# Performance work log

Hardware: AMD Instinct MI355X
Metric: run time of the kernel (lower is better)

## Reference

```python
import jax, jax.numpy as jnp
import numpy as np

B, C, H, W = 2, 256, 64, 64
NH, HD, K = 4, 64, 16  # num_head, head_channel, n_clusters
N = H * W
SCALE = HD ** 0.5


def _lin(x, Wm, b):
    return x @ Wm + b


def _mlp(x, W1, b1, W2, b2):
    h = _lin(x, W1, b1)
    h = jnp.where(h > 0, h, 0.01 * h)  # LeakyReLU(0.01)
    return _lin(h, W2, b2)  # dropout p=0.0 -> identity


def setup_inputs() -> dict:
    key = jax.random.key(0)
    ks = jax.random.split(key, 20)
    s = 1.0 / np.sqrt(C)
    s2 = 1.0 / np.sqrt(2 * C)
    inp = {
        "q_img": jax.random.normal(ks[0], (B, C, H, W), jnp.float32),
        "k_img_map": jax.random.normal(ks[1], (B, C, H, W), jnp.float32),
        "v_img_map": jax.random.normal(ks[2], (B, C, H, W), jnp.float32),
        "labels": jax.random.randint(ks[3], (B, H, W), 0, K),
        "pixel_coefficients": jax.random.uniform(ks[4], (B, N, N), jnp.float32),
        "Wq": jax.random.uniform(ks[5], (C, C), jnp.float32, -s, s),
        "bq": jnp.zeros((C,), jnp.float32),
        "Wk": jax.random.uniform(ks[6], (C, C), jnp.float32, -s, s),
        "bk": jnp.zeros((C,), jnp.float32),
        "Wv": jax.random.uniform(ks[7], (C, C), jnp.float32, -s, s),
        "bv": jnp.zeros((C,), jnp.float32),
        "W11": jax.random.uniform(ks[8], (C, 2 * C), jnp.float32, -s, s),
        "b11": jnp.zeros((2 * C,), jnp.float32),
        "W12": jax.random.uniform(ks[9], (2 * C, C), jnp.float32, -s2, s2),
        "b12": jnp.zeros((C,), jnp.float32),
        "W21": jax.random.uniform(ks[10], (C, 2 * C), jnp.float32, -s, s),
        "b21": jnp.zeros((2 * C,), jnp.float32),
        "W22": jax.random.uniform(ks[11], (2 * C, C), jnp.float32, -s2, s2),
        "b22": jnp.zeros((C,), jnp.float32),
    }
    return inp


def reference(q_img, k_img_map, v_img_map, labels, pixel_coefficients,
              Wq, bq, Wk, bk, Wv, bv, W11, b11, W12, b12, W21, b21, W22, b22):
    # [B,C,H,W] -> [B,N,C]
    q = _lin(q_img.transpose(0, 2, 3, 1).reshape(B, N, C), Wq, bq)
    k = _lin(k_img_map.transpose(0, 2, 3, 1).reshape(B, N, C), Wk, bk)
    v = _lin(v_img_map.transpose(0, 2, 3, 1).reshape(B, N, C), Wv, bv)

    lab = labels.reshape(B, N)
    onehot = (lab[:, :, None] == jnp.arange(K)[None, None, :]).astype(jnp.float32)  # [B,N,K]
    num_k = jnp.einsum('bnk,bnc->bkc', onehot, k)
    den_k = onehot.sum(axis=1)[:, :, None] + 1e-6
    centers_k = num_k / den_k  # [B,K,C]

    qm = q.reshape(B, N, NH, HD).transpose(0, 2, 1, 3)  # [B,h,N,d]
    km = k.reshape(B, N, NH, HD).transpose(0, 2, 1, 3)
    vm = v.reshape(B, N, NH, HD).transpose(0, 2, 1, 3)
    cm = centers_k.reshape(B, K, NH, HD).transpose(0, 2, 1, 3)  # [B,h,K,d]

    attn_intra = jnp.einsum('bhnd,bhmd->bhnm', qm, km)          # [B,h,N,N]
    attn_centers = jnp.einsum('bhnd,bhkd->bhnk', qm, cm)        # [B,h,N,K]

    same = (lab[:, :, None] == lab[:, None, :])[:, None]        # [B,1,N,N]
    idx = jnp.broadcast_to(lab[:, None, None, :], (B, NH, N, N))
    attn_inter = jnp.take_along_axis(attn_centers, idx, axis=-1) * pixel_coefficients[:, None]

    scores = jnp.where(same, attn_intra, attn_inter) / SCALE
    attn = jax.nn.softmax(scores, axis=-1)
    out = jnp.einsum('bhnm,bhmd->bhnd', attn, vm).transpose(0, 2, 1, 3).reshape(B, N, C)

    rs1 = v + _mlp(out, W11, b11, W12, b12)        # [B,N,C] (v_spatial residual)
    rs2 = rs1 + _mlp(rs1, W21, b21, W22, b22)
    return rs2.reshape(B, H, W, C).transpose(0, 3, 1, 2)  # [B,C,H,W]
```

## Files before the change

### kernel.cpp

```cpp
#include <hip/hip_runtime.h>
#include <stdint.h>

#define Bv 2
#define Cv 256
#define Nv 4096
#define NHv 4
#define HDv 64
#define Kv 16


typedef __attribute__((ext_vector_type(8))) short bf16x8;
typedef __attribute__((ext_vector_type(4))) float f32x4;

__device__ __forceinline__ float bf2f(unsigned short u) {
  union { unsigned int i; float f; } x; x.i = ((unsigned int)u) << 16; return x.f;
}
__device__ __forceinline__ unsigned short f2bf(float f) {
  union { float f; unsigned int i; } x; x.f = f;
  unsigned int r = x.i + 0x7FFF + ((x.i >> 16) & 1);
  return (unsigned short)(r >> 16);
}

__global__ __launch_bounds__(256) void imgt_k(
    const float* __restrict__ qi, const float* __restrict__ ki,
    const float* __restrict__ vi, unsigned short* __restrict__ dst)
{
  const int z = blockIdx.z;
  const float* src = (z < 2 ? qi : (z < 4 ? ki : vi)) + (long long)(z & 1) * Cv * Nv;
  unsigned short* out = dst + (long long)z * Nv * Cv;
  __shared__ float t[32][33];
  const int x = threadIdx.x, y = threadIdx.y;
  const int n0 = blockIdx.x * 32, c0 = blockIdx.y * 32;
  for (int i = y; i < 32; i += 8)
    t[i][x] = src[(long long)(c0 + i) * Nv + n0 + x];
  __syncthreads();
  for (int i = y; i < 32; i += 8)
    out[(long long)(n0 + i) * Cv + c0 + x] = f2bf(t[x][i]);
}

struct WP { const float* p[7]; };

__global__ __launch_bounds__(256) void wt_k(WP wp, unsigned short* __restrict__ dst)
{
  const int z = blockIdx.z;
  const int KD[7] = {256, 256, 256, 256, 512, 256, 512};
  const int ND[7] = {256, 256, 256, 512, 256, 512, 256};
  const long long OFF[7] = {0, 65536, 131072, 196608, 327680, 458752, 589824};
  const int Kw = KD[z], Nw = ND[z];
  const int nb = blockIdx.x * 32, kb2 = blockIdx.y * 32;
  if (nb >= Nw || kb2 >= Kw) return;
  __shared__ float t[32][33];
  const int x = threadIdx.x, y = threadIdx.y;
  const float* src = wp.p[z];
  for (int i = y; i < 32; i += 8)
    t[i][x] = src[(long long)(kb2 + i) * Nw + nb + x];
  __syncthreads();
  for (int i = y; i < 32; i += 8)
    dst[OFF[z] + (long long)(nb + i) * Kw + kb2 + x] = f2bf(t[x][i]);
}

__global__ __launch_bounds__(256) void proj_k(
    const unsigned short* __restrict__ imgT, const unsigned short* __restrict__ wt,
    const float* __restrict__ bq, const float* __restrict__ bk, const float* __restrict__ bv,
    unsigned short* __restrict__ qbf, unsigned short* __restrict__ kbf,
    float* __restrict__ vpp, unsigned short* __restrict__ vtb)
{
  __shared__ __align__(16) unsigned short As[128][72];
  __shared__ __align__(16) unsigned short Bs[128][72];
  const int tid = threadIdx.x;
  const int w = tid >> 6, lane = tid & 63;
  const int lr = lane & 15, quad = lane >> 4;
  const int m0 = blockIdx.x * 128, n0 = blockIdx.y * 128;
  const int z = blockIdx.z, zz = z >> 1, bb = z & 1;
  const int wm = (w >> 1) * 64, wn = (w & 1) * 64;
  const int sr = tid >> 1, sh = (tid & 1) * 32;
  const long long NvCv = (long long)Nv * Cv;

  const float* bias = zz == 0 ? bq : (zz == 1 ? bk : bv);
  const unsigned short* Ab0 = imgT + (long long)z * NvCv + (long long)(m0 + sr) * Cv + sh;
  const unsigned short* Bb0 = wt + (long long)zz * 65536 + (long long)(n0 + sr) * Cv + sh;

  f32x4 acc[4][4];
#pragma unroll
  for (int i = 0; i < 4; ++i)
#pragma unroll
    for (int j = 0; j < 4; ++j) acc[i][j] = (f32x4){0.f, 0.f, 0.f, 0.f};

  for (int k0 = 0; k0 < Cv; k0 += 64) {
    const unsigned short* Ab = Ab0 + k0;
    const unsigned short* Bp = Bb0 + k0;
    uint4 a0 = *(const uint4*)Ab, a1 = *(const uint4*)(Ab + 8);
    uint4 a2 = *(const uint4*)(Ab + 16), a3 = *(const uint4*)(Ab + 24);
    uint4 b0 = *(const uint4*)Bp, b1 = *(const uint4*)(Bp + 8);
    uint4 b2 = *(const uint4*)(Bp + 16), b3 = *(const uint4*)(Bp + 24);
    *(uint4*)&As[sr][sh] = a0; *(uint4*)&As[sr][sh + 8] = a1;
    *(uint4*)&As[sr][sh + 16] = a2; *(uint4*)&As[sr][sh + 24] = a3;
    *(uint4*)&Bs[sr][sh] = b0; *(uint4*)&Bs[sr][sh + 8] = b1;
    *(uint4*)&Bs[sr][sh + 16] = b2; *(uint4*)&Bs[sr][sh + 24] = b3;
    __syncthreads();
#pragma unroll
    for (int ks = 0; ks < 2; ++ks) {
      bf16x8 af[4], bfr[4];
#pragma unroll
      for (int i = 0; i < 4; ++i)
        af[i] = *(const bf16x8*)&As[wm + i * 16 + lr][ks * 32 + quad * 8];
#pragma unroll
      for (int j = 0; j < 4; ++j)
        bfr[j] = *(const bf16x8*)&Bs[wn + j * 16 + lr][ks * 32 + quad * 8];
#pragma unroll
      for (int i = 0; i < 4; ++i)
#pragma unroll
        for (int j = 0; j < 4; ++j)
          acc[i][j] = __builtin_amdgcn_mfma_f32_16x16x32_bf16(af[i], bfr[j], acc[i][j], 0, 0, 0);
    }
    __syncthreads();
  }

#pragma unroll
  for (int j = 0; j < 4; ++j) {
    const int col = n0 + wn + j * 16 + lr;
    const float bvv = bias[col];
#pragma unroll
    for (int i = 0; i < 4; ++i) {
      const int mb = m0 + wm + i * 16 + quad * 4;
      float r[4];
#pragma unroll
      for (int reg = 0; reg < 4; ++reg) r[reg] = acc[i][j][reg] + bvv;
      const long long ob = (long long)bb * NvCv;
      if (zz == 0) {
#pragma unroll
        for (int reg = 0; reg < 4; ++reg)
          qbf[ob + (long long)(mb + reg) * Cv + col] = f2bf(r[reg] * 0.125f);
      } else if (zz == 1) {
#pragma unroll
        for (int reg = 0; reg < 4; ++reg)
          kbf[ob + (long long)(mb + reg) * Cv + col] = f2bf(r[reg]);
      } else {
#pragma unroll
        for (int reg = 0; reg < 4; ++reg)
          vpp[ob + (long long)(mb + reg) * Cv + col] = r[reg];
        uint2 pk;
        pk.x = f2bf(r[0]) | ((unsigned int)f2bf(r[1]) << 16);
        pk.y = f2bf(r[2]) | ((unsigned int)f2bf(r[3]) << 16);
        *(uint2*)&vtb[ob + (long long)col * Nv + mb] = pk;
      }
    }
  }
}

template<bool ABF16, int ACT, int RES, int OM>
__global__ __launch_bounds__(256) void mm_k(
    const void* __restrict__ A, const unsigned short* __restrict__ Bt,
    const float* __restrict__ bias, const float* __restrict__ Res,
    float* __restrict__ outF, unsigned short* __restrict__ outB,
    int M, int Nn, int Kd)
{
  __shared__ __align__(16) unsigned short As[128][72];
  __shared__ __align__(16) unsigned short Bs[128][72];
  const int tid = threadIdx.x;
  const int w = tid >> 6, lane = tid & 63;
  const int lr = lane & 15, quad = lane >> 4;
  const int m0 = blockIdx.x * 128, n0 = blockIdx.y * 128;
  const int wm = (w >> 1) * 64, wn = (w & 1) * 64;
  const int sr = tid >> 1, sh = (tid & 1) * 32;

  f32x4 acc[4][4];
#pragma unroll
  for (int i = 0; i < 4; ++i)
#pragma unroll
    for (int j = 0; j < 4; ++j) acc[i][j] = (f32x4){0.f, 0.f, 0.f, 0.f};

  const long long abase = (long long)(m0 + sr) * Kd + sh;
  const unsigned short* Bb = Bt + (long long)(n0 + sr) * Kd + sh;

  for (int k0 = 0; k0 < Kd; k0 += 64) {
    if (ABF16) {
      const unsigned short* Ab = (const unsigned short*)A + abase + k0;
      uint4 u0 = *(const uint4*)Ab, u1 = *(const uint4*)(Ab + 8);
      uint4 u2 = *(const uint4*)(Ab + 16), u3 = *(const uint4*)(Ab + 24);
      *(uint4*)&As[sr][sh] = u0; *(uint4*)&As[sr][sh + 8] = u1;
      *(uint4*)&As[sr][sh + 16] = u2; *(uint4*)&As[sr][sh + 24] = u3;
    } else {
      const float* Af = (const float*)A + abase + k0;
#pragma unroll
      for (int t = 0; t < 4; ++t) {
        const float4 f0 = *(const float4*)(Af + t * 8);
        const float4 f1 = *(const float4*)(Af + t * 8 + 4);
        uint4 pk;
        pk.x = f2bf(f0.x) | ((unsigned int)f2bf(f0.y) << 16);
        pk.y = f2bf(f0.z) | ((unsigned int)f2bf(f0.w) << 16);
        pk.z = f2bf(f1.x) | ((unsigned int)f2bf(f1.y) << 16);
        pk.w = f2bf(f1.z) | ((unsigned int)f2bf(f1.w) << 16);
        *(uint4*)&As[sr][sh + t * 8] = pk;
      }
    }
    {
      const unsigned short* Bp = Bb + k0;
      uint4 u0 = *(const uint4*)Bp, u1 = *(const uint4*)(Bp + 8);
      uint4 u2 = *(const uint4*)(Bp + 16), u3 = *(const uint4*)(Bp + 24);
      *(uint4*)&Bs[sr][sh] = u0; *(uint4*)&Bs[sr][sh + 8] = u1;
      *(uint4*)&Bs[sr][sh + 16] = u2; *(uint4*)&Bs[sr][sh + 24] = u3;
    }
    __syncthreads();
#pragma unroll
    for (int ks = 0; ks < 2; ++ks) {
      bf16x8 af[4], bfr[4];
#pragma unroll
      for (int i = 0; i < 4; ++i)
        af[i] = *(const bf16x8*)&As[wm + i * 16 + lr][ks * 32 + quad * 8];
#pragma unroll
      for (int j = 0; j < 4; ++j)
        bfr[j] = *(const bf16x8*)&Bs[wn + j * 16 + lr][ks * 32 + quad * 8];
#pragma unroll
      for (int i = 0; i < 4; ++i)
#pragma unroll
        for (int j = 0; j < 4; ++j)
          acc[i][j] = __builtin_amdgcn_mfma_f32_16x16x32_bf16(af[i], bfr[j], acc[i][j], 0, 0, 0);
    }
    __syncthreads();
  }

#pragma unroll
  for (int j = 0; j < 4; ++j) {
    const int col = n0 + wn + j * 16 + lr;
    const float bv = bias[col];
#pragma unroll
    for (int i = 0; i < 4; ++i) {
      const int mb = m0 + wm + i * 16 + quad * 4;
      float r[4];
#pragma unroll
      for (int reg = 0; reg < 4; ++reg) {
        float v = acc[i][j][reg] + bv;
        if (ACT) v = v > 0.f ? v : 0.01f * v;
        if (RES) v += Res[(long long)(mb + reg) * Nn + col];
        r[reg] = v;
      }
      if (OM == 0) {
#pragma unroll
        for (int reg = 0; reg < 4; ++reg)
          outF[(long long)(mb + reg) * Nn + col] = r[reg];
      } else if (OM == 1) {
#pragma unroll
        for (int reg = 0; reg < 4; ++reg)
          outB[(long long)(mb + reg) * Nn + col] = f2bf(r[reg]);
      } else {
        const float4 st = {r[0], r[1], r[2], r[3]};
        *(float4*)&outF[((long long)((mb >> 12) * Cv + col)) * Nv + (mb & 4095)] = st;
      }
    }
  }
}

__global__ __launch_bounds__(256) void zero_k(float* p, int n)
{
  const int i = blockIdx.x * 256 + threadIdx.x;
  if (i < n) p[i] = 0.f;
}

__global__ __launch_bounds__(256) void center_accum(
    const unsigned short* __restrict__ kb, const int* __restrict__ labels,
    float* __restrict__ cent, float* __restrict__ cnts)
{
  __shared__ int lab_s[512];
  const int bx = blockIdx.x;
  const int chunk = bx & 7;
  const int kk = (bx >> 3) & 15;
  const int b = bx >> 7;
  const int c = threadIdx.x;
  const int nbase = chunk * 512;
  for (int i = threadIdx.x; i < 512; i += 256) lab_s[i] = labels[b * Nv + nbase + i];
  __syncthreads();
  float acc = 0.f;
  int cnt = 0;
#pragma unroll 4
  for (int i = 0; i < 512; ++i) {
    if (lab_s[i] == kk) {
      acc += bf2f(kb[(long long)(b * Nv + nbase + i) * Cv + c]);
      ++cnt;
    }
  }
  atomicAdd(&cent[(b * Kv + kk) * Cv + c], acc);
  if (c == 0) atomicAdd(&cnts[b * Kv + kk], (float)cnt);
}

__global__ __launch_bounds__(256) void center_norm(float* cent, const float* cnts)
{
  const int i = blockIdx.x * 256 + threadIdx.x;
  cent[i] = cent[i] / (cnts[i >> 8] + 1e-6f);
}

union PSCS {
  unsigned short p[4][16][68];
  float c[16][68];
};

__global__ __launch_bounds__(256) void attn_k(
    const unsigned short* __restrict__ qb, const unsigned short* __restrict__ kb,
    const unsigned short* __restrict__ vtb, const float* __restrict__ cent,
    const int* __restrict__ labels, const float* __restrict__ pc,
    float* __restrict__ opart, float* __restrict__ lpart)
{
  __shared__ __align__(16) unsigned short q_s[64][72];
  __shared__ __align__(16) unsigned short k_s[64][72];
  __shared__ __align__(16) unsigned short vt_s[64][72];
  __shared__ __align__(16) PSCS u_s;
  __shared__ float ac_s[64][17];

  const int tid = threadIdx.x;
  const int lane = tid & 63, w = tid >> 6;
  const int lr = lane & 15, quad = lane >> 4;
  const int bx = blockIdx.x;
  const int qt = bx & 63, h = (bx >> 6) & 3, b = (bx >> 8) & 1;
  const int part = bx >> 9;
  const int n0 = qt * 64;
  const int mbase = part * 2048;
  const int sr2 = tid >> 2, so2 = (tid & 3) * 16;
  const int row_l = w * 16 + quad * 4;
  const long long pcb = (long long)b * Nv * Nv;

  {
    const unsigned short* src = qb + ((long long)(b * Nv + n0 + sr2)) * Cv + h * HDv + so2;
    *(uint4*)&q_s[sr2][so2] = *(const uint4*)src;
    *(uint4*)&q_s[sr2][so2 + 8] = *(const uint4*)(src + 8);
  }
  for (int idx = tid; idx < Kv * HDv; idx += 256)
    u_s.c[idx >> 6][idx & 63] = cent[((long long)(b * Kv + (idx >> 6))) * Cv + h * HDv + (idx & 63)];

  uint4 ka0, ka1, va0, va1;
  float pc1[4][4];
  int labm1[4], labq[4];
  {
    const long long ks = ((long long)(b * Nv + mbase + sr2)) * Cv + h * HDv + so2;
    ka0 = *(const uint4*)(kb + ks); ka1 = *(const uint4*)(kb + ks + 8);
    const long long vs = ((long long)(b * Cv + h * HDv + sr2)) * Nv + mbase + so2;
    va0 = *(const uint4*)(vtb + vs); va1 = *(const uint4*)(vtb + vs + 8);
  }
#pragma unroll
  for (int sub = 0; sub < 4; ++sub) {
    labm1[sub] = labels[b * Nv + mbase + sub * 16 + lr];
#pragma unroll
    for (int reg = 0; reg < 4; ++reg)
      pc1[sub][reg] = pc[pcb + (long long)(n0 + row_l + reg) * Nv + mbase + sub * 16 + lr];
  }
#pragma unroll
  for (int reg = 0; reg < 4; ++reg) labq[reg] = labels[b * Nv + n0 + row_l + reg];

  __syncthreads();
  for (int idx = tid; idx < 64 * Kv; idx += 256) {
    const int r = idx >> 4, kk = idx & 15;
    float s = 0.f;
#pragma unroll
    for (int d = 0; d < HDv; ++d) s += bf2f(q_s[r][d]) * u_s.c[kk][d];
    ac_s[r][kk] = s;
  }
  const bf16x8 qa0 = *(const bf16x8*)&q_s[w * 16 + lr][quad * 8];
  const bf16x8 qa1 = *(const bf16x8*)&q_s[w * 16 + lr][32 + quad * 8];
  __syncthreads();

  *(uint4*)&k_s[sr2][so2] = ka0; *(uint4*)&k_s[sr2][so2 + 8] = ka1;
  *(uint4*)&vt_s[sr2][so2] = va0; *(uint4*)&vt_s[sr2][so2 + 8] = va1;
  __syncthreads();

  f32x4 oacc[4];
#pragma unroll
  for (int s2 = 0; s2 < 4; ++s2) oacc[s2] = (f32x4){0.f, 0.f, 0.f, 0.f};
  float lrow[4] = {0.f, 0.f, 0.f, 0.f};

  for (int t = 0; t < 32; ++t) {
    const int m0 = mbase + t * 64;
    const bool has = (t < 31);

    if (has) {
      const long long ks = ((long long)(b * Nv + m0 + 64 + sr2)) * Cv + h * HDv + so2;
      ka0 = *(const uint4*)(kb + ks); ka1 = *(const uint4*)(kb + ks + 8);
      const long long vs = ((long long)(b * Cv + h * HDv + sr2)) * Nv + m0 + 64 + so2;
      va0 = *(const uint4*)(vtb + vs); va1 = *(const uint4*)(vtb + vs + 8);
    }

    f32x4 sacc[4];
#pragma unroll
    for (int sub = 0; sub < 4; ++sub) {
      const bf16x8 kb0 = *(const bf16x8*)&k_s[sub * 16 + lr][quad * 8];
      const bf16x8 kb1 = *(const bf16x8*)&k_s[sub * 16 + lr][32 + quad * 8];
      f32x4 s = (f32x4){0.f, 0.f, 0.f, 0.f};
      s = __builtin_amdgcn_mfma_f32_16x16x32_bf16(qa0, kb0, s, 0, 0, 0);
      s = __builtin_amdgcn_mfma_f32_16x16x32_bf16(qa1, kb1, s, 0, 0, 0);
      sacc[sub] = s;
    }

#pragma unroll
    for (int reg = 0; reg < 4; ++reg) {
      const int Ln = labq[reg];
#pragma unroll
      for (int sub = 0; sub < 4; ++sub) {
        const float s = (labm1[sub] == Ln) ? sacc[sub][reg]
                                           : ac_s[row_l + reg][labm1[sub]] * pc1[sub][reg];
        const float p = __expf(s - 4.0f);
        lrow[reg] += p;
        u_s.p[w][quad * 4 + reg][sub * 16 + lr] = f2bf(p);
      }
    }

    if (has) {
#pragma unroll
      for (int sub = 0; sub < 4; ++sub) {
        labm1[sub] = labels[b * Nv + m0 + 64 + sub * 16 + lr];
#pragma unroll
        for (int reg = 0; reg < 4; ++reg)
          pc1[sub][reg] = pc[pcb + (long long)(n0 + row_l + reg) * Nv + m0 + 64 + sub * 16 + lr];
      }
    }

    const bf16x8 pa0 = *(const bf16x8*)&u_s.p[w][lr][quad * 8];
    const bf16x8 pa1 = *(const bf16x8*)&u_s.p[w][lr][32 + quad * 8];
#pragma unroll
    for (int sub = 0; sub < 4; ++sub) {
      const bf16x8 vb0 = *(const bf16x8*)&vt_s[sub * 16 + lr][quad * 8];
      const bf16x8 vb1 = *(const bf16x8*)&vt_s[sub * 16 + lr][32 + quad * 8];
      oacc[sub] = __builtin_amdgcn_mfma_f32_16x16x32_bf16(pa0, vb0, oacc[sub], 0, 0, 0);
      oacc[sub] = __builtin_amdgcn_mfma_f32_16x16x32_bf16(pa1, vb1, oacc[sub], 0, 0, 0);
    }

    __syncthreads();
    if (has) {
      *(uint4*)&k_s[sr2][so2] = ka0; *(uint4*)&k_s[sr2][so2 + 8] = ka1;
      *(uint4*)&vt_s[sr2][so2] = va0; *(uint4*)&vt_s[sr2][so2 + 8] = va1;
    }
    __syncthreads();
  }

#pragma unroll
  for (int reg = 0; reg < 4; ++reg) {
    float l = lrow[reg];
    l += __shfl_xor(l, 1); l += __shfl_xor(l, 2);
    l += __shfl_xor(l, 4); l += __shfl_xor(l, 8);
    const int row = n0 + row_l + reg;
    const long long obase = (long long)part * 2097152 + ((long long)(b * Nv + row)) * Cv + h * HDv;
#pragma unroll
    for (int sub = 0; sub < 4; ++sub)
      opart[obase + sub * 16 + lr] = oacc[sub][reg];
    if (lr == 0)
      lpart[part * 32768 + (b * 4 + h) * 4096 + row] = l;
  }
}

__global__ __launch_bounds__(256) void combine_k(
    const float* __restrict__ op, const float* __restrict__ lp,
    unsigned short* __restrict__ aob)
{
  const long long i4 = ((long long)blockIdx.x * 256 + threadIdx.x) * 4;
  const int c = (int)(i4 & 255), n = (int)((i4 >> 8) & 4095), b = (int)(i4 >> 20);
  const int h = c >> 6;
  const float l = lp[(b * 4 + h) * 4096 + n] + lp[32768 + (b * 4 + h) * 4096 + n];
  const float inv = 1.f / l;
  const float4 a = *(const float4*)&op[i4];
  const float4 d = *(const float4*)&op[2097152 + i4];
  uint2 pk;
  pk.x = f2bf((a.x + d.x) * inv) | ((unsigned int)f2bf((a.y + d.y) * inv) << 16);
  pk.y = f2bf((a.z + d.z) * inv) | ((unsigned int)f2bf((a.w + d.w) * inv) << 16);
  *(uint2*)&aob[i4] = pk;
}

extern "C" void kernel_launch(void* const* d_in, const int* in_sizes, int n_in,
                              void* d_out, int out_size, void* d_ws, size_t ws_size,
                              hipStream_t stream)
{
  const float* q_img = (const float*)d_in[0];
  const float* k_img = (const float*)d_in[1];
  const float* v_img = (const float*)d_in[2];
  const int* labels  = (const int*)d_in[3];
  const float* pc    = (const float*)d_in[4];
  const float* Wq  = (const float*)d_in[5];  const float* bq  = (const float*)d_in[6];
  const float* Wk  = (const float*)d_in[7];  const float* bk  = (const float*)d_in[8];
  const float* Wv  = (const float*)d_in[9];  const float* bv  = (const float*)d_in[10];
  const float* W11 = (const float*)d_in[11]; const float* b11 = (const float*)d_in[12];
  const float* W12 = (const float*)d_in[13]; const float* b12 = (const float*)d_in[14];
  const float* W21 = (const float*)d_in[15]; const float* b21 = (const float*)d_in[16];
  const float* W22 = (const float*)d_in[17]; const float* b22 = (const float*)d_in[18];
  float* outp = (float*)d_out;

  const long long SZ = (long long)Bv * Nv * Cv;
  float* ws    = (float*)d_ws;
  float* vpp   = ws;
  float* rs1   = vpp + SZ;
  float* opart = rs1 + SZ;
  float* lpart = opart + 2 * SZ;
  float* cent  = lpart + 65536;
  float* cnts  = cent + Bv * Kv * Cv;
  unsigned short* wt   = (unsigned short*)(cnts + Bv * Kv);
  unsigned short* qbf  = wt + 720896;
  unsigned short* kbf  = qbf + SZ;
  unsigned short* vtb  = kbf + SZ;
  unsigned short* aob  = vtb + SZ;
  unsigned short* h1b  = aob + SZ;
  unsigned short* imgT = aob;

  imgt_k<<<dim3(Nv / 32, Cv / 32, 6), dim3(32, 8), 0, stream>>>(q_img, k_img, v_img, imgT);
  WP wp = {{Wq, Wk, Wv, W11, W12, W21, W22}};
  wt_k<<<dim3(16, 16, 7), dim3(32, 8), 0, stream>>>(wp, wt);

  proj_k<<<dim3(32, 2, 6), 256, 0, stream>>>(imgT, wt, bq, bk, bv, qbf, kbf, vpp, vtb);

  zero_k<<<dim3(33), 256, 0, stream>>>(cent, Bv * Kv * Cv + Bv * Kv);
  center_accum<<<dim3(Bv * Kv * 8), 256, 0, stream>>>(kbf, labels, cent, cnts);
  center_norm<<<dim3(Bv * Kv * Cv / 256), 256, 0, stream>>>(cent, cnts);

  attn_k<<<dim3(1024), 256, 0, stream>>>(qbf, kbf, vtb, cent, labels, pc, opart, lpart);
  combine_k<<<dim3(2048), 256, 0, stream>>>(opart, lpart, aob);

  mm_k<true, 1, 0, 1><<<dim3(64, 4), 256, 0, stream>>>(
      aob, wt + 196608, b11, nullptr, nullptr, h1b, 2 * Nv, 2 * Cv, Cv);
  mm_k<true, 0, 1, 0><<<dim3(64, 2), 256, 0, stream>>>(
      h1b, wt + 327680, b12, vpp, rs1, nullptr, 2 * Nv, Cv, 2 * Cv);

  mm_k<false, 1, 0, 1><<<dim3(64, 4), 256, 0, stream>>>(
      rs1, wt + 458752, b21, nullptr, nullptr, h1b, 2 * Nv, 2 * Cv, Cv);
  mm_k<true, 0, 1, 4><<<dim3(64, 2), 256, 0, stream>>>(
      h1b, wt + 589824, b22, rs1, outp, nullptr, 2 * Nv, Cv, 2 * Cv);
}
```

Before: 447.9 us.

## Split attention keys across warps with in-block combine, shrink MLP GEMM tiles

After: 640.9 us. +43.1%, slower.

```diff
diff --git a/kernel.cpp b/kernel.cpp
--- a/kernel.cpp
+++ b/kernel.cpp
@@ -130,7 +130,7 @@
       if (zz == 0) {
 #pragma unroll
         for (int reg = 0; reg < 4; ++reg)
-          qbf[ob + (long long)(mb + reg) * Cv + col] = f2bf(r[reg] * 0.125f);
+          qbf[ob + (long long)(mb + reg) * Cv + col] = f2bf(r[reg] * 0.18033688f);
       } else if (zz == 1) {
 #pragma unroll
         for (int reg = 0; reg < 4; ++reg)
@@ -149,26 +149,26 @@
 }
 
 template<bool ABF16, int ACT, int RES, int OM>
-__global__ __launch_bounds__(256) void mm_k(
+__global__ __launch_bounds__(256) void mm64_k(
     const void* __restrict__ A, const unsigned short* __restrict__ Bt,
     const float* __restrict__ bias, const float* __restrict__ Res,
     float* __restrict__ outF, unsigned short* __restrict__ outB,
     int M, int Nn, int Kd)
 {
-  __shared__ __align__(16) unsigned short As[128][72];
-  __shared__ __align__(16) unsigned short Bs[128][72];
+  __shared__ __align__(16) unsigned short As[64][72];
+  __shared__ __align__(16) unsigned short Bs[64][72];
   const int tid = threadIdx.x;
   const int w = tid >> 6, lane = tid & 63;
   const int lr = lane & 15, quad = lane >> 4;
-  const int m0 = blockIdx.x * 128, n0 = blockIdx.y * 128;
-  const int wm = (w >> 1) * 64, wn = (w & 1) * 64;
-  const int sr = tid >> 1, sh = (tid & 1) * 32;
-
-  f32x4 acc[4][4];
-#pragma unroll
-  for (int i = 0; i < 4; ++i)
-#pragma unroll
-    for (int j = 0; j < 4; ++j) acc[i][j] = (f32x4){0.f, 0.f, 0.f, 0.f};
+  const int m0 = blockIdx.x * 64, n0 = blockIdx.y * 64;
+  const int wm = (w >> 1) * 32, wn = (w & 1) * 32;
+  const int sr = tid >> 2, sh = (tid & 3) * 16;
+
+  f32x4 acc[2][2];
+#pragma unroll
+  for (int i = 0; i < 2; ++i)
+#pragma unroll
+    for (int j = 0; j < 2; ++j) acc[i][j] = (f32x4){0.f, 0.f, 0.f, 0.f};
 
   const long long abase = (long long)(m0 + sr) * Kd + sh;
   const unsigned short* Bb = Bt + (long long)(n0 + sr) * Kd + sh;
@@ -177,13 +177,11 @@
     if (ABF16) {
       const unsigned short* Ab = (const unsigned short*)A + abase + k0;
       uint4 u0 = *(const uint4*)Ab, u1 = *(const uint4*)(Ab + 8);
-      uint4 u2 = *(const uint4*)(Ab + 16), u3 = *(const uint4*)(Ab + 24);
       *(uint4*)&As[sr][sh] = u0; *(uint4*)&As[sr][sh + 8] = u1;
-      *(uint4*)&As[sr][sh + 16] = u2; *(uint4*)&As[sr][sh + 24] = u3;
     } else {
       const float* Af = (const float*)A + abase + k0;
 #pragma unroll
-      for (int t = 0; t < 4; ++t) {
+      for (int t = 0; t < 2; ++t) {
         const float4 f0 = *(const float4*)(Af + t * 8);
         const float4 f1 = *(const float4*)(Af + t * 8 + 4);
         uint4 pk;
@@ -197,35 +195,33 @@
     {
       const unsigned short* Bp = Bb + k0;
       uint4 u0 = *(const uint4*)Bp, u1 = *(const uint4*)(Bp + 8);
-      uint4 u2 = *(const uint4*)(Bp + 16), u3 = *(const uint4*)(Bp + 24);
       *(uint4*)&Bs[sr][sh] = u0; *(uint4*)&Bs[sr][sh + 8] = u1;
-      *(uint4*)&Bs[sr][sh + 16] = u2; *(uint4*)&Bs[sr][sh + 24] = u3;
     }
     __syncthreads();
 #pragma unroll
     for (int ks = 0; ks < 2; ++ks) {
-      bf16x8 af[4], bfr[4];
-#pragma unroll
-      for (int i = 0; i < 4; ++i)
+      bf16x8 af[2], bfr[2];
+#pragma unroll
+      for (int i = 0; i < 2; ++i)
         af[i] = *(const bf16x8*)&As[wm + i * 16 + lr][ks * 32 + quad * 8];
 #pragma unroll
-      for (int j = 0; j < 4; ++j)
+      for (int j = 0; j < 2; ++j)
         bfr[j] = *(const bf16x8*)&Bs[wn + j * 16 + lr][ks * 32 + quad * 8];
 #pragma unroll
-      for (int i = 0; i < 4; ++i)
-#pragma unroll
-        for (int j = 0; j < 4; ++j)
+      for (int i = 0; i < 2; ++i)
+#pragma unroll
+        for (int j = 0; j < 2; ++j)
           acc[i][j] = __builtin_amdgcn_mfma_f32_16x16x32_bf16(af[i], bfr[j], acc[i][j], 0, 0, 0);
     }
     __syncthreads();
   }
 
 #pragma unroll
-  for (int j = 0; j < 4; ++j) {
+  for (int j = 0; j < 2; ++j) {
     const int col = n0 + wn + j * 16 + lr;
     const float bv = bias[col];
 #pragma unroll
-    for (int i = 0; i < 4; ++i) {
+    for (int i = 0; i < 2; ++i) {
       const int mb = m0 + wm + i * 16 + quad * 4;
       float r[4];
 #pragma unroll
@@ -289,76 +285,63 @@
   cent[i] = cent[i] / (cnts[i >> 8] + 1e-6f);
 }
 
-union PSCS {
-  unsigned short p[4][16][68];
-  float c[16][68];
-};
-
 __global__ __launch_bounds__(256) void attn_k(
     const unsigned short* __restrict__ qb, const unsigned short* __restrict__ kb,
     const unsigned short* __restrict__ vtb, const float* __restrict__ cent,
     const int* __restrict__ labels, const float* __restrict__ pc,
-    float* __restrict__ opart, float* __restrict__ lpart)
-{
-  __shared__ __align__(16) unsigned short q_s[64][72];
-  __shared__ __align__(16) unsigned short k_s[64][72];
-  __shared__ __align__(16) unsigned short vt_s[64][72];
-  __shared__ __align__(16) PSCS u_s;
-  __shared__ float ac_s[64][17];
+    unsigned short* __restrict__ aob)
+{
+  __shared__ __align__(16) unsigned short p_s[4][16][68];
+  __shared__ float ac_s[16][17];
+  __shared__ float combO[16][68];
+  __shared__ float combL[16];
 
   const int tid = threadIdx.x;
   const int lane = tid & 63, w = tid >> 6;
   const int lr = lane & 15, quad = lane >> 4;
   const int bx = blockIdx.x;
-  const int qt = bx & 63, h = (bx >> 6) & 3, b = (bx >> 8) & 1;
-  const int part = bx >> 9;
-  const int n0 = qt * 64;
-  const int mbase = part * 2048;
-  const int sr2 = tid >> 2, so2 = (tid & 3) * 16;
-  const int row_l = w * 16 + quad * 4;
-  const long long pcb = (long long)b * Nv * Nv;
+  const int h = bx & 3, qt = (bx >> 2) & 255, b = bx >> 10;
+  const int n0 = qt * 16;
+  const int row4 = quad * 4;
+
+  const unsigned short* qp = qb + ((long long)(b * Nv + n0 + lr)) * Cv + h * HDv + quad * 8;
+  const bf16x8 qa0 = *(const bf16x8*)qp;
+  const bf16x8 qa1 = *(const bf16x8*)(qp + 32);
+
+  const unsigned short* kwp = kb + ((long long)(b * Nv + w * 64 + lr)) * Cv + h * HDv + quad * 8;
+  const unsigned short* vwp = vtb + ((long long)(b * Cv + h * HDv + lr)) * Nv + w * 64 + quad * 8;
+  const float* pcw = pc + (long long)b * Nv * Nv + (long long)(n0 + row4) * Nv + w * 64 + lr;
+  const int* lbw = labels + b * Nv + w * 64 + lr;
 
   {
-    const unsigned short* src = qb + ((long long)(b * Nv + n0 + sr2)) * Cv + h * HDv + so2;
-    *(uint4*)&q_s[sr2][so2] = *(const uint4*)src;
-    *(uint4*)&q_s[sr2][so2 + 8] = *(const uint4*)(src + 8);
-  }
-  for (int idx = tid; idx < Kv * HDv; idx += 256)
-    u_s.c[idx >> 6][idx & 63] = cent[((long long)(b * Kv + (idx >> 6))) * Cv + h * HDv + (idx & 63)];
-
-  uint4 ka0, ka1, va0, va1;
-  float pc1[4][4];
-  int labm1[4], labq[4];
-  {
-    const long long ks = ((long long)(b * Nv + mbase + sr2)) * Cv + h * HDv + so2;
-    ka0 = *(const uint4*)(kb + ks); ka1 = *(const uint4*)(kb + ks + 8);
-    const long long vs = ((long long)(b * Cv + h * HDv + sr2)) * Nv + mbase + so2;
-    va0 = *(const uint4*)(vtb + vs); va1 = *(const uint4*)(vtb + vs + 8);
-  }
+    const int r = tid >> 4, kk = tid & 15;
+    const unsigned short* qr = qb + ((long long)(b * Nv + n0 + r)) * Cv + h * HDv;
+    const float* cr = cent + ((long long)(b * Kv + kk)) * Cv + h * HDv;
+    float s0 = 0.f, s1 = 0.f, s2 = 0.f, s3 = 0.f;
+#pragma unroll
+    for (int d = 0; d < HDv; d += 4) {
+      s0 += bf2f(qr[d]) * cr[d];
+      s1 += bf2f(qr[d + 1]) * cr[d + 1];
+      s2 += bf2f(qr[d + 2]) * cr[d + 2];
+      s3 += bf2f(qr[d + 3]) * cr[d + 3];
+    }
+    ac_s[r][kk] = (s0 + s1) + (s2 + s3);
+  }
+
+  int labq[4];
+#pragma unroll
+  for (int reg = 0; reg < 4; ++reg) labq[reg] = labels[b * Nv + n0 + row4 + reg];
+
+  float pcv[4][4];
+  int labm[4];
 #pragma unroll
   for (int sub = 0; sub < 4; ++sub) {
-    labm1[sub] = labels[b * Nv + mbase + sub * 16 + lr];
+    labm[sub] = lbw[sub * 16];
 #pragma unroll
     for (int reg = 0; reg < 4; ++reg)
-      pc1[sub][reg] = pc[pcb + (long long)(n0 + row_l + reg) * Nv + mbase + sub * 16 + lr];
-  }
-#pragma unroll
-  for (int reg = 0; reg < 4; ++reg) labq[reg] = labels[b * Nv + n0 + row_l + reg];
-
-  __syncthreads();
-  for (int idx = tid; idx < 64 * Kv; idx += 256) {
-    const int r = idx >> 4, kk = idx & 15;
-    float s = 0.f;
-#pragma unroll
-    for (int d = 0; d < HDv; ++d) s += bf2f(q_s[r][d]) * u_s.c[kk][d];
-    ac_s[r][kk] = s;
-  }
-  const bf16x8 qa0 = *(const bf16x8*)&q_s[w * 16 + lr][quad * 8];
-  const bf16x8 qa1 = *(const bf16x8*)&q_s[w * 16 + lr][32 + quad * 8];
-  __syncthreads();
-
-  *(uint4*)&k_s[sr2][so2] = ka0; *(uint4*)&k_s[sr2][so2 + 8] = ka1;
-  *(uint4*)&vt_s[sr2][so2] = va0; *(uint4*)&vt_s[sr2][so2 + 8] = va1;
+      pcv[sub][reg] = pcw[(long long)reg * Nv + sub * 16];
+  }
+
   __syncthreads();
 
   f32x4 oacc[4];
@@ -366,25 +349,18 @@
   for (int s2 = 0; s2 < 4; ++s2) oacc[s2] = (f32x4){0.f, 0.f, 0.f, 0.f};
   float lrow[4] = {0.f, 0.f, 0.f, 0.f};
 
-  for (int t = 0; t < 32; ++t) {
-    const int m0 = mbase + t * 64;
-    const bool has = (t < 31);
-
-    if (has) {
-      const long long ks = ((long long)(b * Nv + m0 + 64 + sr2)) * Cv + h * HDv + so2;
-      ka0 = *(const uint4*)(kb + ks); ka1 = *(const uint4*)(kb + ks + 8);
-      const long long vs = ((long long)(b * Cv + h * HDv + sr2)) * Nv + m0 + 64 + so2;
-      va0 = *(const uint4*)(vtb + vs); va1 = *(const uint4*)(vtb + vs + 8);
-    }
+  for (int tt = 0; tt < 16; ++tt) {
+    const unsigned short* kt = kwp + (long long)tt * (256 * Cv);
+    const unsigned short* vt = vwp + tt * 256;
 
     f32x4 sacc[4];
 #pragma unroll
     for (int sub = 0; sub < 4; ++sub) {
-      const bf16x8 kb0 = *(const bf16x8*)&k_s[sub * 16 + lr][quad * 8];
-      const bf16x8 kb1 = *(const bf16x8*)&k_s[sub * 16 + lr][32 + quad * 8];
+      const bf16x8 k0v = *(const bf16x8*)(kt + sub * (16 * Cv));
+      const bf16x8 k1v = *(const bf16x8*)(kt + sub * (16 * Cv) + 32);
       f32x4 s = (f32x4){0.f, 0.f, 0.f, 0.f};
-      s = __builtin_amdgcn_mfma_f32_16x16x32_bf16(qa0, kb0, s, 0, 0, 0);
-      s = __builtin_amdgcn_mfma_f32_16x16x32_bf16(qa1, kb1, s, 0, 0, 0);
+      s = __builtin_amdgcn_mfma_f32_16x16x32_bf16(qa0, k0v, s, 0, 0, 0);
+      s = __builtin_amdgcn_mfma_f32_16x16x32_bf16(qa1, k1v, s, 0, 0, 0);
       sacc[sub] = s;
     }
 
@@ -393,72 +369,68 @@
       const int Ln = labq[reg];
 #pragma unroll
       for (int sub = 0; sub < 4; ++sub) {
-        const float s = (labm1[sub] == Ln) ? sacc[sub][reg]
-                                           : ac_s[row_l + reg][labm1[sub]] * pc1[sub][reg];
-        const float p = __expf(s - 4.0f);
+        const float s = (labm[sub] == Ln) ? sacc[sub][reg]
+                                          : ac_s[row4 + reg][labm[sub]] * pcv[sub][reg];
+        const float p = exp2f(s - 5.770780f);
         lrow[reg] += p;
-        u_s.p[w][quad * 4 + reg][sub * 16 + lr] = f2bf(p);
-      }
-    }
-
-    if (has) {
+        p_s[w][row4 + reg][sub * 16 + lr] = f2bf(p);
+      }
+    }
+
+    if (tt < 15) {
+      const int off = (tt + 1) * 256;
 #pragma unroll
       for (int sub = 0; sub < 4; ++sub) {
-        labm1[sub] = labels[b * Nv + m0 + 64 + sub * 16 + lr];
-#pragma unroll
-        for (int reg = 0; reg < 4; ++reg)
-          pc1[sub][reg] = pc[pcb + (long long)(n0 + row_l + reg) * Nv + m0 + 64 + sub * 16 + lr];
-      }
-    }
-
-    const bf16x8 pa0 = *(const bf16x8*)&u_s.p[w][lr][quad * 8];
-    const bf16x8 pa1 = *(const bf16x8*)&u_s.p[w][lr][32 + quad * 8];
+        labm[sub] = lbw[off + sub * 16];
+#pragma unroll
+        for (int reg = 0; reg < 4; ++reg)
+          pcv[sub][reg] = pcw[(long long)reg * Nv + off + sub * 16];
+      }
+    }
+
+    const bf16x8 pa0 = *(const bf16x8*)&p_s[w][lr][quad * 8];
+    const bf16x8 pa1 = *(const bf16x8*)&p_s[w][lr][32 + quad * 8];
 #pragma unroll
     for (int sub = 0; sub < 4; ++sub) {
-      const bf16x8 vb0 = *(const bf16x8*)&vt_s[sub * 16 + lr][quad * 8];
-      const bf16x8 vb1 = *(const bf16x8*)&vt_s[sub * 16 + lr][32 + quad * 8];
-      oacc[sub] = __builtin_amdgcn_mfma_f32_16x16x32_bf16(pa0, vb0, oacc[sub], 0, 0, 0);
-      oacc[sub] = __builtin_amdgcn_mfma_f32_16x16x32_bf16(pa1, vb1, oacc[sub], 0, 0, 0);
-    }
-
-    __syncthreads();
-    if (has) {
-      *(uint4*)&k_s[sr2][so2] = ka0; *(uint4*)&k_s[sr2][so2 + 8] = ka1;
-      *(uint4*)&vt_s[sr2][so2] = va0; *(uint4*)&vt_s[sr2][so2 + 8] = va1;
-    }
-    __syncthreads();
+      const bf16x8 v0v = *(const bf16x8*)(vt + (long long)sub * (16 * Nv));
+      const bf16x8 v1v = *(const bf16x8*)(vt + (long long)sub * (16 * Nv) + 32);
+      oacc[sub] = __builtin_amdgcn_mfma_f32_16x16x32_bf16(pa0, v0v, oacc[sub], 0, 0, 0);
+      oacc[sub] = __builtin_amdgcn_mfma_f32_16x16x32_bf16(pa1, v1v, oacc[sub], 0, 0, 0);
+    }
   }
 
 #pragma unroll
   for (int reg = 0; reg < 4; ++reg) {
-    float l = lrow[reg];
-    l += __shfl_xor(l, 1); l += __shfl_xor(l, 2);
-    l += __shfl_xor(l, 4); l += __shfl_xor(l, 8);
-    const int row = n0 + row_l + reg;
-    const long long obase = (long long)part * 2097152 + ((long long)(b * Nv + row)) * Cv + h * HDv;
-#pragma unroll
-    for (int sub = 0; sub < 4; ++sub)
-      opart[obase + sub * 16 + lr] = oacc[sub][reg];
-    if (lr == 0)
-      lpart[part * 32768 + (b * 4 + h) * 4096 + row] = l;
-  }
-}
-
-__global__ __launch_bounds__(256) void combine_k(
-    const float* __restrict__ op, const float* __restrict__ lp,
-    unsigned short* __restrict__ aob)
-{
-  const long long i4 = ((long long)blockIdx.x * 256 + threadIdx.x) * 4;
-  const int c = (int)(i4 & 255), n = (int)((i4 >> 8) & 4095), b = (int)(i4 >> 20);
-  const int h = c >> 6;
-  const float l = lp[(b * 4 + h) * 4096 + n] + lp[32768 + (b * 4 + h) * 4096 + n];
-  const float inv = 1.f / l;
-  const float4 a = *(const float4*)&op[i4];
-  const float4 d = *(const float4*)&op[2097152 + i4];
-  uint2 pk;
-  pk.x = f2bf((a.x + d.x) * inv) | ((unsigned int)f2bf((a.y + d.y) * inv) << 16);
-  pk.y = f2bf((a.z + d.z) * inv) | ((unsigned int)f2bf((a.w + d.w) * inv) << 16);
-  *(uint2*)&aob[i4] = pk;
+    lrow[reg] += __shfl_xor(lrow[reg], 1);
+    lrow[reg] += __shfl_xor(lrow[reg], 2);
+    lrow[reg] += __shfl_xor(lrow[reg], 4);
+    lrow[reg] += __shfl_xor(lrow[reg], 8);
+  }
+
+  for (int i = tid; i < 16 * 68; i += 256) (&combO[0][0])[i] = 0.f;
+  if (tid < 16) combL[tid] = 0.f;
+  __syncthreads();
+#pragma unroll
+  for (int sub = 0; sub < 4; ++sub)
+#pragma unroll
+    for (int reg = 0; reg < 4; ++reg)
+      atomicAdd(&combO[row4 + reg][sub * 16 + lr], oacc[sub][reg]);
+  if (lr == 0) {
+#pragma unroll
+    for (int reg = 0; reg < 4; ++reg) atomicAdd(&combL[row4 + reg], lrow[reg]);
+  }
+  __syncthreads();
+
+  {
+    const int row = tid >> 4, c4 = (tid & 15) * 4;
+    const float inv = 1.f / combL[row];
+    const float o0 = combO[row][c4] * inv, o1 = combO[row][c4 + 1] * inv;
+    const float o2 = combO[row][c4 + 2] * inv, o3 = combO[row][c4 + 3] * inv;
+    uint2 pk;
+    pk.x = f2bf(o0) | ((unsigned int)f2bf(o1) << 16);
+    pk.y = f2bf(o2) | ((unsigned int)f2bf(o3) << 16);
+    *(uint2*)&aob[((long long)(b * Nv + n0 + row)) * Cv + h * HDv + c4] = pk;
+  }
 }
 
 extern "C" void kernel_launch(void* const* d_in, const int* in_sizes, int n_in,
@@ -483,9 +455,7 @@
   float* ws    = (float*)d_ws;
   float* vpp   = ws;
   float* rs1   = vpp + SZ;
-  float* opart = rs1 + SZ;
-  float* lpart = opart + 2 * SZ;
-  float* cent  = lpart + 65536;
+  float* cent  = rs1 + SZ;
   float* cnts  = cent + Bv * Kv * Cv;
   unsigned short* wt   = (unsigned short*)(cnts + Bv * Kv);
   unsigned short* qbf  = wt + 720896;
@@ -505,16 +475,15 @@
   center_accum<<<dim3(Bv * Kv * 8), 256, 0, stream>>>(kbf, labels, cent, cnts);
   center_norm<<<dim3(Bv * Kv * Cv / 256), 256, 0, stream>>>(cent, cnts);
 
-  attn_k<<<dim3(1024), 256, 0, stream>>>(qbf, kbf, vtb, cent, labels, pc, opart, lpart);
-  combine_k<<<dim3(2048), 256, 0, stream>>>(opart, lpart, aob);
-
-  mm_k<true, 1, 0, 1><<<dim3(64, 4), 256, 0, stream>>>(
+  attn_k<<<dim3(2048), 256, 0, stream>>>(qbf, kbf, vtb, cent, labels, pc, aob);
+
+  mm64_k<true, 1, 0, 1><<<dim3(128, 8), 256, 0, stream>>>(
       aob, wt + 196608, b11, nullptr, nullptr, h1b, 2 * Nv, 2 * Cv, Cv);
-  mm_k<true, 0, 1, 0><<<dim3(64, 2), 256, 0, stream>>>(
+  mm64_k<true, 0, 1, 0><<<dim3(128, 4), 256, 0, stream>>>(
       h1b, wt + 327680, b12, vpp, rs1, nullptr, 2 * Nv, Cv, 2 * Cv);
 
-  mm_k<false, 1, 0, 1><<<dim3(64, 4), 256, 0, stream>>>(
+  mm64_k<false, 1, 0, 1><<<dim3(128, 8), 256, 0, stream>>>(
       rs1, wt + 458752, b21, nullptr, nullptr, h1b, 2 * Nv, 2 * Cv, Cv);
-  mm_k<true, 0, 1, 4><<<dim3(64, 2), 256, 0, stream>>>(
+  mm64_k<true, 0, 1, 4><<<dim3(128, 4), 256, 0, stream>>>(
       h1b, wt + 589824, b22, rs1, outp, nullptr, 2 * Nv, Cv, 2 * Cv);
 }
```
